# Optimization experiments

Measured on AMD Instinct MI355X. Metric: run time of the kernel, lower is better.

## Reference

```python
import jax, jax.numpy as jnp
import numpy as np

BATCH, SEQ, DIM, NH = 4, 2048, 1024, 16
HD = DIM // NH  # 64

def _rope_cos_sin(seq_len, head_dim, dtype=jnp.float32):
    inv_freq = 1.0 / (10000.0 ** (jnp.arange(0, head_dim, 2, dtype=dtype) / head_dim))
    t = jnp.arange(seq_len, dtype=dtype)
    freqs = jnp.outer(t, inv_freq)                # (seq, hd/2)
    emb = jnp.concatenate([freqs, freqs], axis=-1)  # (seq, hd)
    return jnp.cos(emb), jnp.sin(emb)

def _apply_rope(x, cos, sin):
    # x: (b, h, s, d); cos/sin: (s, d)
    d2 = x.shape[-1] // 2
    x1, x2 = x[..., :d2], x[..., d2:]
    c = cos[None, None, :, :d2]
    s = sin[None, None, :, :d2]
    return jnp.concatenate([x1 * c - x2 * s, x1 * s + x2 * c], axis=-1)

def setup_inputs() -> dict:
    key = jax.random.key(0)
    ks = jax.random.split(key, 3)
    x = jax.random.normal(ks[0], (BATCH, SEQ, DIM), dtype=jnp.float32)
    Wqkv = jax.random.normal(ks[1], (DIM, 3 * DIM), dtype=jnp.float32) * (1.0 / np.sqrt(DIM))
    bqkv = jnp.zeros((3 * DIM,), dtype=jnp.float32)
    Wout = jax.random.normal(ks[2], (DIM, DIM), dtype=jnp.float32) * (1.0 / np.sqrt(DIM))
    bout = jnp.zeros((DIM,), dtype=jnp.float32)
    return {"x": x, "Wqkv": Wqkv, "bqkv": bqkv, "Wout": Wout, "bout": bout}

def reference(x, Wqkv, bqkv, Wout, bout):
    b, s, dim = x.shape
    qkv = x @ Wqkv + bqkv                          # (b, s, 3*dim)
    qkv = qkv.reshape(b, s, 3, NH, HD).transpose(2, 0, 3, 1, 4)  # (3, b, h, s, hd)
    q, k, v = qkv[0], qkv[1], qkv[2]
    cos, sin = _rope_cos_sin(s, HD, x.dtype)
    q = _apply_rope(q, cos, sin)
    k = _apply_rope(k, cos, sin)
    scale = HD ** -0.5
    scores = jnp.einsum('bhqd,bhkd->bhqk', q, k) * scale
    attn = jax.nn.softmax(scores, axis=-1)
    attn = jnp.nan_to_num(attn, nan=0.0)
    out = jnp.einsum('bhqk,bhkd->bhqd', attn, v)   # (b, h, s, hd)
    out = out.transpose(0, 2, 1, 3).reshape(b, s, dim)
    return out @ Wout + bout
```

## Files before the change

kernel.cpp:

```cpp
#include <hip/hip_runtime.h>
#include <hip/hip_bf16.h>
#include <stdint.h>

#define DEVI __device__ __forceinline__

typedef __attribute__((ext_vector_type(8))) short bf16x8;
typedef __attribute__((ext_vector_type(4))) float f32x4;

DEVI float bf2f(short u) {
  union { unsigned int i; float f; } v;
  v.i = ((unsigned int)(unsigned short)u) << 16;
  return v.f;
}
DEVI short f2bf(float f) {
  union { float f; unsigned int i; } v; v.f = f;
  unsigned int r = v.i + 0x7FFFu + ((v.i >> 16) & 1u);
  return (short)(r >> 16);
}

DEVI bf16x8 ldsfrag(const short* t, int row, int k0) {
  int slot = k0 >> 3;
  return *(const bf16x8*)(t + row * 64 + ((slot ^ (row & 7)) << 3));
}

DEVI void gload16(const void* g, void* l) {
  __builtin_amdgcn_global_load_lds((const __attribute__((address_space(1))) void*)g,
                                   (__attribute__((address_space(3))) void*)l, 16, 0, 0);
}

__global__ void k_cvt(const float* __restrict__ in, short* __restrict__ out, int n4) {
  int i = blockIdx.x * blockDim.x + threadIdx.x;
  if (i >= n4) return;
  float4 v = ((const float4*)in)[i];
  short4 o;
  o.x = f2bf(v.x); o.y = f2bf(v.y); o.z = f2bf(v.z); o.w = f2bf(v.w);
  ((short4*)out)[i] = o;
}

__global__ void k_transpose_bf16(const float* __restrict__ in, short* __restrict__ outp,
                                 int R, int C) {
  __shared__ float tile[32][33];
  const int c0 = blockIdx.x * 32, r0 = blockIdx.y * 32;
  const int tx = threadIdx.x, ty = threadIdx.y;
  for (int i = ty; i < 32; i += 8) tile[i][tx] = in[(size_t)(r0 + i) * C + c0 + tx];
  __syncthreads();
  for (int i = ty; i < 32; i += 8) outp[(size_t)(c0 + i) * R + r0 + tx] = f2bf(tile[tx][i]);
}

__global__ void k_rope(float* __restrict__ cosTt, float* __restrict__ sinTt) {
  int idx = blockIdx.x * blockDim.x + threadIdx.x;
  int i = idx >> 11, s = idx & 2047;
  float inv = exp2f(-0.41524101186092034f * (float)i);
  float f = (float)s * inv;
  cosTt[idx] = cosf(f);
  sinTt[idx] = sinf(f);
}

__global__ __launch_bounds__(256) void k_gemm_qkv(const short* __restrict__ A,
                                                  const short* __restrict__ BT,
                                                  const float* __restrict__ bias,
                                                  const float* __restrict__ cosTt,
                                                  const float* __restrict__ sinTt,
                                                  short* __restrict__ qo,
                                                  short* __restrict__ ko,
                                                  short* __restrict__ vp) {
  __shared__ __align__(16) short smem[17408];
  short* As = smem;
  short* Bs = smem + 8192;
  const int tid = threadIdx.x;
  const int lane = tid & 63, wid = tid >> 6;
  const int ln = lane & 15, grp = lane >> 4;
  const int wm = wid >> 1, wn = wid & 1;
  const int bx = blockIdx.x;
  const int r0 = blockIdx.y * 128, c0 = bx * 128;
  const int K = 1024;

  const short* aSrc[4];
  const short* bSrc[4];
  int ldst[4];
#pragma unroll
  for (int j = 0; j < 4; ++j) {
    int chunk = wid * 256 + j * 64 + lane;
    int row = chunk >> 3, gs = (chunk & 7) ^ (row & 7);
    aSrc[j] = A + (size_t)(r0 + row) * K + gs * 8;
    bSrc[j] = BT + (size_t)(c0 + row) * K + gs * 8;
    ldst[j] = (wid * 256 + j * 64) * 8;
  }

  f32x4 acc[4][4];
#pragma unroll
  for (int i = 0; i < 4; ++i)
#pragma unroll
    for (int j = 0; j < 4; ++j) acc[i][j] = (f32x4){0.f, 0.f, 0.f, 0.f};

  for (int kt = 0; kt < 16; ++kt) {
    __syncthreads();
#pragma unroll
    for (int j = 0; j < 4; ++j) {
      gload16(aSrc[j], &As[ldst[j]]);
      gload16(bSrc[j], &Bs[ldst[j]]);
      aSrc[j] += 64;
      bSrc[j] += 64;
    }
    __syncthreads();
#pragma unroll
    for (int ks = 0; ks < 2; ++ks) {
      const int k0 = ks * 32 + grp * 8;
      bf16x8 af[4], bfr[4];
#pragma unroll
      for (int mi = 0; mi < 4; ++mi) af[mi] = ldsfrag(As, wm * 64 + mi * 16 + ln, k0);
#pragma unroll
      for (int ni = 0; ni < 4; ++ni) bfr[ni] = ldsfrag(Bs, wn * 64 + ni * 16 + ln, k0);
#pragma unroll
      for (int mi = 0; mi < 4; ++mi)
#pragma unroll
        for (int ni = 0; ni < 4; ++ni)
          acc[mi][ni] = __builtin_amdgcn_mfma_f32_16x16x32_bf16(af[mi], bfr[ni], acc[mi][ni], 0, 0, 0);
    }
  }

  __syncthreads();
  const int third = bx >> 3;
  const int h0 = (bx & 7) * 2;
  const int b = r0 >> 11, sb = r0 & 2047;

  if (third < 2) {
    const float QS = (third == 0) ? 0.18033688011112042f : 1.0f;
#pragma unroll
    for (int mi = 0; mi < 4; ++mi) {
      const int s0 = sb + wm * 64 + mi * 16 + grp * 4;
      const int rowb = (wm * 64 + mi * 16 + grp * 4) * 136 + wn * 64;
#pragma unroll
      for (int ni = 0; ni < 2; ++ni) {
        const int d1 = ni * 16 + ln;
        float4 cv = *(const float4*)(cosTt + d1 * 2048 + s0);
        float4 sv = *(const float4*)(sinTt + d1 * 2048 + s0);
        const float b1 = bias[c0 + wn * 64 + d1];
        const float b2 = bias[c0 + wn * 64 + d1 + 32];
#pragma unroll
        for (int r = 0; r < 4; ++r) {
          float x1 = acc[mi][ni][r] + b1;
          float x2 = acc[mi][ni + 2][r] + b2;
          float c = ((const float*)&cv)[r], s = ((const float*)&sv)[r];
          smem[rowb + r * 136 + d1]      = f2bf((x1 * c - x2 * s) * QS);
          smem[rowb + r * 136 + d1 + 32] = f2bf((x1 * s + x2 * c) * QS);
        }
      }
    }
    __syncthreads();
    const int rloc = tid >> 1, ph = tid & 1;
    const int bh = b * 16 + h0 + ph;
    short* dst = (third == 0 ? qo : ko) + ((size_t)bh * 2048 + sb + rloc) * 64;
    const short* src = smem + rloc * 136 + ph * 64;
#pragma unroll
    for (int j = 0; j < 8; ++j) *(int4*)(dst + j * 8) = *(const int4*)(src + j * 8);
  } else {
#pragma unroll
    for (int mi = 0; mi < 4; ++mi) {
      const int rowb = (wm * 64 + mi * 16 + grp * 4) * 136 + wn * 64;
#pragma unroll
      for (int ni = 0; ni < 4; ++ni) {
        const float bv = bias[c0 + wn * 64 + ni * 16 + ln];
#pragma unroll
        for (int r = 0; r < 4; ++r)
          smem[rowb + r * 136 + ni * 16 + ln] = f2bf(acc[mi][ni][r] + bv);
      }
    }
    __syncthreads();
#pragma unroll
    for (int i = 0; i < 8; ++i) {
      const int g = i * 256 + tid;
      const int ph = g >> 10, tt = (g >> 9) & 1, cc2 = g & 511;
      const int ks = cc2 >> 8, mi = (cc2 >> 6) & 3, grp_ = (cc2 >> 4) & 3, ln_ = cc2 & 15;
      const int d = mi * 16 + ln_;
      bf16x8 o;
#pragma unroll
      for (int e = 0; e < 8; ++e) {
        const int key = tt * 64 + 32 * ks + 16 * (e >> 2) + 4 * grp_ + (e & 3);
        o[e] = smem[key * 136 + ph * 64 + d];
      }
      const int bh = b * 16 + h0 + ph;
      const int tg = (sb >> 6) + tt;
      *(bf16x8*)(vp + ((size_t)bh * 32 + tg) * 4096 + cc2 * 8) = o;
    }
  }
}

__global__ __launch_bounds__(256) void k_gemm_out(const short* __restrict__ A,
                                                  const short* __restrict__ BT,
                                                  const float* __restrict__ bias,
                                                  float* __restrict__ outp,
                                                  int M, int N, int K) {
  __shared__ __align__(16) short As[128 * 64];
  __shared__ __align__(16) short Bs[128 * 64];
  const int tid = threadIdx.x;
  const int lane = tid & 63, wid = tid >> 6;
  const int ln = lane & 15, grp = lane >> 4;
  const int wm = wid >> 1, wn = wid & 1;
  const int r0 = blockIdx.y * 128, c0 = blockIdx.x * 128;

  const short* aSrc[4];
  const short* bSrc[4];
  int ldst[4];
#pragma unroll
  for (int j = 0; j < 4; ++j) {
    int chunk = wid * 256 + j * 64 + lane;
    int row = chunk >> 3, gs = (chunk & 7) ^ (row & 7);
    aSrc[j] = A + (size_t)(r0 + row) * K + gs * 8;
    bSrc[j] = BT + (size_t)(c0 + row) * K + gs * 8;
    ldst[j] = (wid * 256 + j * 64) * 8;
  }

  f32x4 acc[4][4];
#pragma unroll
  for (int i = 0; i < 4; ++i)
#pragma unroll
    for (int j = 0; j < 4; ++j) acc[i][j] = (f32x4){0.f, 0.f, 0.f, 0.f};

  const int nkt = K >> 6;
  for (int kt = 0; kt < nkt; ++kt) {
    __syncthreads();
#pragma unroll
    for (int j = 0; j < 4; ++j) {
      gload16(aSrc[j], &As[ldst[j]]);
      gload16(bSrc[j], &Bs[ldst[j]]);
      aSrc[j] += 64;
      bSrc[j] += 64;
    }
    __syncthreads();
#pragma unroll
    for (int ks = 0; ks < 2; ++ks) {
      const int k0 = ks * 32 + grp * 8;
      bf16x8 af[4], bfr[4];
#pragma unroll
      for (int mi = 0; mi < 4; ++mi) af[mi] = ldsfrag(As, wm * 64 + mi * 16 + ln, k0);
#pragma unroll
      for (int ni = 0; ni < 4; ++ni) bfr[ni] = ldsfrag(Bs, wn * 64 + ni * 16 + ln, k0);
#pragma unroll
      for (int mi = 0; mi < 4; ++mi)
#pragma unroll
        for (int ni = 0; ni < 4; ++ni)
          acc[mi][ni] = __builtin_amdgcn_mfma_f32_16x16x32_bf16(af[mi], bfr[ni], acc[mi][ni], 0, 0, 0);
    }
  }
#pragma unroll
  for (int ni = 0; ni < 4; ++ni) {
    const int col = c0 + wn * 64 + ni * 16 + ln;
    const float bv = bias[col];
#pragma unroll
    for (int mi = 0; mi < 4; ++mi) {
#pragma unroll
      for (int r = 0; r < 4; ++r) {
        const int rowg = r0 + wm * 64 + mi * 16 + grp * 4 + r;
        outp[(size_t)rowg * N + col] = acc[mi][ni][r] + bv;
      }
    }
  }
}

__global__ __launch_bounds__(256) void k_attn(const short* __restrict__ Q,
                                              const short* __restrict__ Kk,
                                              const short* __restrict__ Vp,
                                              short* __restrict__ out) {
  __shared__ __align__(16) short smem[2 * 8192];
  const int tid = threadIdx.x;
  const int lane = tid & 63, wid = tid >> 6;
  const int ln = lane & 15, grp = lane >> 4;
  const int qt = blockIdx.x, bh = blockIdx.y;
  const int b = bh >> 4, h = bh & 15;

  bf16x8 qf[2][2];
#pragma unroll
  for (int g = 0; g < 2; ++g)
#pragma unroll
    for (int ks = 0; ks < 2; ++ks)
      qf[g][ks] = *(const bf16x8*)(Q + ((size_t)bh * 2048 + qt * 128 + wid * 32 + g * 16 + ln) * 64
                                   + ks * 32 + grp * 8);

  const short* kSrc0;
  const short* kSrc1;
  const short* vSrc0;
  const short* vSrc1;
  int ldk0, ldk1, ldv0, ldv1;
  {
    int c0i = wid * 64 + lane;
    int r0i = c0i >> 3, g0i = (c0i & 7) ^ (r0i & 7);
    kSrc0 = Kk + (size_t)bh * 2048 * 64 + (size_t)r0i * 64 + g0i * 8;
    ldk0 = wid * 512;
    int c1i = 256 + wid * 64 + lane;
    int r1i = c1i >> 3, g1i = (c1i & 7) ^ (r1i & 7);
    kSrc1 = Kk + (size_t)bh * 2048 * 64 + (size_t)r1i * 64 + g1i * 8;
    ldk1 = 2048 + wid * 512;
    const short* vt = Vp + (size_t)bh * 32 * 4096;
    vSrc0 = vt + (size_t)c0i * 8;
    ldv0 = 4096 + wid * 512;
    vSrc1 = vt + (size_t)c1i * 8;
    ldv1 = 4096 + 2048 + wid * 512;
  }

  f32x4 acc[2][4];
  f32x4 accl[2];
#pragma unroll
  for (int g = 0; g < 2; ++g) {
    accl[g] = (f32x4){0.f, 0.f, 0.f, 0.f};
#pragma unroll
    for (int i = 0; i < 4; ++i) acc[g][i] = (f32x4){0.f, 0.f, 0.f, 0.f};
  }
  bf16x8 ones;
#pragma unroll
  for (int e = 0; e < 8; ++e) ones[e] = (short)0x3F80;

  union PU { bf16x8 v; unsigned int u[4]; };

  gload16(kSrc0, &smem[ldk0]);
  gload16(kSrc1, &smem[ldk1]);
  gload16(vSrc0, &smem[ldv0]);
  gload16(vSrc1, &smem[ldv1]);
  kSrc0 += 4096; kSrc1 += 4096; vSrc0 += 4096; vSrc1 += 4096;
  __syncthreads();

  int cur = 0;
  for (int t = 0; t < 32; ++t) {
    if (t < 31) {
      const int bo = (cur ^ 1) * 8192;
      gload16(kSrc0, &smem[bo + ldk0]);
      gload16(kSrc1, &smem[bo + ldk1]);
      gload16(vSrc0, &smem[bo + ldv0]);
      gload16(vSrc1, &smem[bo + ldv1]);
      kSrc0 += 4096; kSrc1 += 4096; vSrc0 += 4096; vSrc1 += 4096;
    }
    const short* Kb = smem + cur * 8192;
    const short* Vb = Kb + 4096;

    f32x4 sf[2][4];
#pragma unroll
    for (int g = 0; g < 2; ++g)
#pragma unroll
      for (int ni = 0; ni < 4; ++ni) sf[g][ni] = (f32x4){0.f, 0.f, 0.f, 0.f};
#pragma unroll
    for (int ks = 0; ks < 2; ++ks) {
      bf16x8 kf[4];
#pragma unroll
      for (int ni = 0; ni < 4; ++ni) kf[ni] = ldsfrag(Kb, ni * 16 + ln, ks * 32 + grp * 8);
      __builtin_amdgcn_s_setprio(1);
#pragma unroll
      for (int g = 0; g < 2; ++g)
#pragma unroll
        for (int ni = 0; ni < 4; ++ni)
          sf[g][ni] = __builtin_amdgcn_mfma_f32_16x16x32_bf16(kf[ni], qf[g][ks], sf[g][ni], 0, 0, 0);
      __builtin_amdgcn_s_setprio(0);
    }

    PU pbf[2][2];
#pragma unroll
    for (int g = 0; g < 2; ++g) {
#pragma unroll
      for (int ni = 0; ni < 4; ++ni) {
        f32x4 s = sf[g][ni];
#pragma unroll
        for (int r = 0; r < 4; ++r) s[r] = __builtin_amdgcn_exp2f(s[r]);
        sf[g][ni] = s;
      }
#pragma unroll
      for (int ks = 0; ks < 2; ++ks)
#pragma unroll
        for (int j = 0; j < 4; ++j) {
          float lo = sf[g][2 * ks + (j >> 1)][(j & 1) * 2];
          float hi = sf[g][2 * ks + (j >> 1)][(j & 1) * 2 + 1];
          unsigned int rr;
          asm("v_cvt_pk_bf16_f32 %0, %1, %2" : "=v"(rr) : "v"(lo), "v"(hi));
          pbf[g][ks].u[j] = rr;
        }
    }

#pragma unroll
    for (int ks = 0; ks < 2; ++ks) {
      bf16x8 vf[4];
#pragma unroll
      for (int mi = 0; mi < 4; ++mi)
        vf[mi] = *(const bf16x8*)(Vb + (ks * 256 + mi * 64 + lane) * 8);
      __builtin_amdgcn_s_setprio(1);
#pragma unroll
      for (int g = 0; g < 2; ++g) {
#pragma unroll
        for (int mi = 0; mi < 4; ++mi)
          acc[g][mi] = __builtin_amdgcn_mfma_f32_16x16x32_bf16(vf[mi], pbf[g][ks].v, acc[g][mi], 0, 0, 0);
        accl[g] = __builtin_amdgcn_mfma_f32_16x16x32_bf16(ones, pbf[g][ks].v, accl[g], 0, 0, 0);
      }
      __builtin_amdgcn_s_setprio(0);
    }

    __syncthreads();
    cur ^= 1;
  }

#pragma unroll
  for (int g = 0; g < 2; ++g) {
    const float inv = 1.0f / accl[g][0];
    const int q = wid * 32 + g * 16 + ln;
#pragma unroll
    for (int mi = 0; mi < 4; ++mi) {
      short4 p;
      p.x = f2bf(acc[g][mi][0] * inv);
      p.y = f2bf(acc[g][mi][1] * inv);
      p.z = f2bf(acc[g][mi][2] * inv);
      p.w = f2bf(acc[g][mi][3] * inv);
      int slot = mi * 2 + (grp >> 1);
      *(short4*)(&smem[q * 64 + ((slot ^ (q & 7)) << 3) + (grp & 1) * 4]) = p;
    }
  }
  __syncthreads();
  {
    const int row = tid >> 1, half = tid & 1;
#pragma unroll
    for (int j = 0; j < 4; ++j) {
      int c = half * 4 + j;
      int4 v = *(const int4*)(&smem[row * 64 + ((c ^ (row & 7)) << 3)]);
      *(int4*)(out + ((size_t)b * 2048 + qt * 128 + row) * 1024 + h * 64 + c * 8) = v;
    }
  }
}

extern "C" void kernel_launch(void* const* d_in, const int* in_sizes, int n_in,
                              void* d_out, int out_size, void* d_ws, size_t ws_size,
                              hipStream_t stream) {
  const float* x    = (const float*)d_in[0];
  const float* Wqkv = (const float*)d_in[1];
  const float* bqkv = (const float*)d_in[2];
  const float* Wout = (const float*)d_in[3];
  const float* bout = (const float*)d_in[4];
  float* out = (float*)d_out;

  char* p = (char*)d_ws;
  short* xb    = (short*)p; p += (size_t)8192 * 1024 * 2;
  short* wqkvT = (short*)p; p += (size_t)3072 * 1024 * 2;
  short* woutT = (short*)p; p += (size_t)1024 * 1024 * 2;
  float* cosTt = (float*)p; p += (size_t)32 * 2048 * 4;
  float* sinTt = (float*)p; p += (size_t)32 * 2048 * 4;
  short* qb    = (short*)p; p += (size_t)64 * 2048 * 64 * 2;
  short* kb    = (short*)p; p += (size_t)64 * 2048 * 64 * 2;
  short* vpb   = (short*)p; p += (size_t)64 * 2048 * 64 * 2;
  short* ao    = (short*)p; p += (size_t)8192 * 1024 * 2;

  k_cvt<<<8192 * 1024 / 4 / 256, 256, 0, stream>>>(x, xb, 8192 * 1024 / 4);
  k_transpose_bf16<<<dim3(3072 / 32, 1024 / 32), dim3(32, 8), 0, stream>>>(Wqkv, wqkvT, 1024, 3072);
  k_transpose_bf16<<<dim3(1024 / 32, 1024 / 32), dim3(32, 8), 0, stream>>>(Wout, woutT, 1024, 1024);
  k_rope<<<32 * 2048 / 256, 256, 0, stream>>>(cosTt, sinTt);
  k_gemm_qkv<<<dim3(24, 64), 256, 0, stream>>>(xb, wqkvT, bqkv, cosTt, sinTt, qb, kb, vpb);
  k_attn<<<dim3(16, 64), 256, 0, stream>>>(qb, kb, vpb, ao);
  k_gemm_out<<<dim3(1024 / 128, 8192 / 128), 256, 0, stream>>>(ao, woutT, bout, out,
                                                               8192, 1024, 1024);
}
```

Before: 207.4 us.

## Swizzle block order for XCD locality and single-buffer attention K/V tiles

Remaps the linear block index in all three main kernels so that consecutive blocks on the same XCD (round-robin by 8) handle neighbouring tiles. This is meant to improve L2 reuse of shared A/B or K/V data. The attention kernel also drops double-buffered LDS in favour of a single buffer with two barriers per iteration. That halves LDS use, which may raise occupancy, but it gives up overlap between the global loads and the MFMA work.

```diff
diff --git a/kernel.cpp b/kernel.cpp
--- a/kernel.cpp
+++ b/kernel.cpp
@@ -71,8 +71,10 @@
   const int lane = tid & 63, wid = tid >> 6;
   const int ln = lane & 15, grp = lane >> 4;
   const int wm = wid >> 1, wn = wid & 1;
-  const int bx = blockIdx.x;
-  const int r0 = blockIdx.y * 128, c0 = bx * 128;
+  const int L = blockIdx.y * 24 + blockIdx.x;
+  const int W = (L & 7) * 192 + (L >> 3);
+  const int bx = W % 24;
+  const int r0 = (W / 24) * 128, c0 = bx * 128;
   const int K = 1024;
 
   const short* aSrc[4];
@@ -197,7 +199,9 @@
   const int lane = tid & 63, wid = tid >> 6;
   const int ln = lane & 15, grp = lane >> 4;
   const int wm = wid >> 1, wn = wid & 1;
-  const int r0 = blockIdx.y * 128, c0 = blockIdx.x * 128;
+  const int L = blockIdx.y * 8 + blockIdx.x;
+  const int W = (L & 7) * 64 + (L >> 3);
+  const int r0 = (W >> 3) * 128, c0 = (W & 7) * 128;
 
   const short* aSrc[4];
   const short* bSrc[4];
@@ -262,11 +266,13 @@
                                               const short* __restrict__ Kk,
                                               const short* __restrict__ Vp,
                                               short* __restrict__ out) {
-  __shared__ __align__(16) short smem[2 * 8192];
+  __shared__ __align__(16) short smem[8192];
   const int tid = threadIdx.x;
   const int lane = tid & 63, wid = tid >> 6;
   const int ln = lane & 15, grp = lane >> 4;
-  const int qt = blockIdx.x, bh = blockIdx.y;
+  const int L = blockIdx.y * 16 + blockIdx.x;
+  const int W = (L & 7) * 128 + (L >> 3);
+  const int qt = W & 15, bh = W >> 4;
   const int b = bh >> 4, h = bh & 15;
 
   bf16x8 qf[2][2];
@@ -312,25 +318,16 @@
 
   union PU { bf16x8 v; unsigned int u[4]; };
 
-  gload16(kSrc0, &smem[ldk0]);
-  gload16(kSrc1, &smem[ldk1]);
-  gload16(vSrc0, &smem[ldv0]);
-  gload16(vSrc1, &smem[ldv1]);
-  kSrc0 += 4096; kSrc1 += 4096; vSrc0 += 4096; vSrc1 += 4096;
-  __syncthreads();
-
-  int cur = 0;
   for (int t = 0; t < 32; ++t) {
-    if (t < 31) {
-      const int bo = (cur ^ 1) * 8192;
-      gload16(kSrc0, &smem[bo + ldk0]);
-      gload16(kSrc1, &smem[bo + ldk1]);
-      gload16(vSrc0, &smem[bo + ldv0]);
-      gload16(vSrc1, &smem[bo + ldv1]);
-      kSrc0 += 4096; kSrc1 += 4096; vSrc0 += 4096; vSrc1 += 4096;
-    }
-    const short* Kb = smem + cur * 8192;
-    const short* Vb = Kb + 4096;
+    __syncthreads();
+    gload16(kSrc0, &smem[ldk0]);
+    gload16(kSrc1, &smem[ldk1]);
+    gload16(vSrc0, &smem[ldv0]);
+    gload16(vSrc1, &smem[ldv1]);
+    kSrc0 += 4096; kSrc1 += 4096; vSrc0 += 4096; vSrc1 += 4096;
+    __syncthreads();
+    const short* Kb = smem;
+    const short* Vb = smem + 4096;
 
     f32x4 sf[2][4];
 #pragma unroll
@@ -389,11 +386,9 @@
       }
       __builtin_amdgcn_s_setprio(0);
     }
-
-    __syncthreads();
-    cur ^= 1;
-  }
-
+  }
+
+  __syncthreads();
 #pragma unroll
   for (int g = 0; g < 2; ++g) {
     const float inv = 1.0f / accl[g][0];
@@ -448,6 +443,6 @@
   k_rope<<<32 * 2048 / 256, 256, 0, stream>>>(cosTt, sinTt);
   k_gemm_qkv<<<dim3(24, 64), 256, 0, stream>>>(xb, wqkvT, bqkv, cosTt, sinTt, qb, kb, vpb);
   k_attn<<<dim3(16, 64), 256, 0, stream>>>(qb, kb, vpb, ao);
-  k_gemm_out<<<dim3(1024 / 128, 8192 / 128), 256, 0, stream>>>(ao, woutT, bout, out,
-                                                               8192, 1024, 1024);
-}
+  k_gemm_out<<<dim3(8, 64), 256, 0, stream>>>(ao, woutT, bout, out,
+                                              8192, 1024, 1024);
+}
```

New measurement: 213.0 us. +2.7%, slower.
